# Kernel tuning notes

Measured on AMD Instinct MI355X. Metric: run time of the kernel, lower is better.

The kernel has to match this reference:

```python
import jax, jax.numpy as jnp
import numpy as np

B, S, D = 2, 2048, 2048
H, KV, HD = 16, 4, 128          # n_heads, n_kv_heads, head_dim = d_model // n_heads
R = H // KV                      # n_rep (GQA group size)
THETA = 500000.0


def _rotate_half(x):
    x1, x2 = jnp.split(x, 2, axis=-1)
    return jnp.concatenate([-x2, x1], axis=-1)


def _rope_cos_sin(position_ids):
    # inv_freq over even dims, outer with positions, duplicated (LLaMA-style)
    inv_freq = 1.0 / (THETA ** (jnp.arange(0, HD, 2, dtype=jnp.float32) / HD))
    freqs = position_ids.astype(jnp.float32)[..., None] * inv_freq  # (B, S, HD/2)
    emb = jnp.concatenate([freqs, freqs], axis=-1)                  # (B, S, HD)
    return jnp.cos(emb)[:, None], jnp.sin(emb)[:, None]             # (B, 1, S, HD)


def setup_inputs() -> dict:
    key = jax.random.key(0)
    ks = jax.random.split(key, 5)
    x = jax.random.normal(ks[0], (B, S, D), dtype=jnp.float32)
    wq = jax.random.normal(ks[1], (D, H * HD), dtype=jnp.float32) * (D ** -0.5)
    wk = jax.random.normal(ks[2], (D, KV * HD), dtype=jnp.float32) * (D ** -0.5)
    wv = jax.random.normal(ks[3], (D, KV * HD), dtype=jnp.float32) * (D ** -0.5)
    wo = jax.random.normal(ks[4], (H * HD, D), dtype=jnp.float32) * (D ** -0.5)
    causal = jnp.tril(jnp.ones((S, S), dtype=bool))
    attn_mask = jnp.where(causal, 0.0, -1e9).astype(jnp.float32)[None, None]  # (1,1,S,S)
    position_ids = jnp.tile(jnp.arange(S, dtype=jnp.int32)[None, :], (B, 1))
    return {"x": x, "wq": wq, "wk": wk, "wv": wv, "wo": wo,
            "attn_mask": attn_mask, "position_ids": position_ids}


def reference(x, wq, wk, wv, wo, attn_mask, position_ids):
    b, s, _ = x.shape
    # projections (bias-free Linear) + head split, (B, heads, S, HD)
    q = (x @ wq).reshape(b, s, H, HD).transpose(0, 2, 1, 3)
    k = (x @ wk).reshape(b, s, KV, HD).transpose(0, 2, 1, 3)
    v = (x @ wv).reshape(b, s, KV, HD).transpose(0, 2, 1, 3)
    cos, sin = _rope_cos_sin(position_ids)
    q = q * cos + _rotate_half(q) * sin
    k = k * cos + _rotate_half(k) * sin
    # GQA: group q heads (B, KV, R, S, HD); equivalent to repeat_interleave on K/V
    qg = q.reshape(b, KV, R, s, HD)
    scores = jnp.einsum('bgrsd,bgtd->bgrst', qg.astype(jnp.float32),
                        k.astype(jnp.float32)) / np.float32(np.sqrt(HD))
    scores = scores + attn_mask[:, :, None]          # (1,1,1,S,S) broadcast
    p = jax.nn.softmax(scores, axis=-1).astype(x.dtype)
    out = jnp.einsum('bgrst,bgtd->bgrsd', p, v)      # (B, KV, R, S, HD)
    out = out.reshape(b, H, s, HD).transpose(0, 2, 1, 3).reshape(b, s, H * HD)
    return out @ wo
```

## Files before the change

### kernel.cpp

```cpp
#include <hip/hip_runtime.h>
#include <hip/hip_bf16.h>
#include <math.h>

#define Bsz 2
#define Sq  2048
#define Dm  2048
#define Hn  16
#define KVn 4
#define HDn 128

typedef __attribute__((ext_vector_type(8))) short bf16x8;
typedef __attribute__((ext_vector_type(4))) float f32x4;

__device__ __forceinline__ short f2b(float f) {
    __hip_bfloat16 h = __float2bfloat16(f);
    return *reinterpret_cast<short*>(&h);
}
__device__ __forceinline__ float b2f(short s) {
    __hip_bfloat16 h = *reinterpret_cast<__hip_bfloat16*>(&s);
    return __bfloat162float(h);
}

__global__ __launch_bounds__(256) void f2b_kernel(
    const float* __restrict__ X, short* __restrict__ Y, int n4)
{
    int i = blockIdx.x * 256 + threadIdx.x;
    if (i >= n4) return;
    float4 v = ((const float4*)X)[i];
    short4 o;
    o.x = f2b(v.x); o.y = f2b(v.y); o.z = f2b(v.z); o.w = f2b(v.w);
    ((short4*)Y)[i] = o;
}

__global__ __launch_bounds__(256) void wconv_all_kernel(
    const float* __restrict__ wq, const float* __restrict__ wk,
    const float* __restrict__ wv, const float* __restrict__ wo,
    short* __restrict__ wqkvT, short* __restrict__ woT)
{
    __shared__ float t[32][33];
    const int n0 = blockIdx.x * 32;
    const int k0 = blockIdx.y * 32;
    const int tx = threadIdx.x, ty = threadIdx.y;

    const float* W; int Nsec, nloc; short* dst;
    if (n0 < 2048)      { W = wq; Nsec = 2048; nloc = n0;        dst = wqkvT + (size_t)n0 * Dm; }
    else if (n0 < 2560) { W = wk; Nsec = 512;  nloc = n0 - 2048; dst = wqkvT + (size_t)n0 * Dm; }
    else if (n0 < 3072) { W = wv; Nsec = 512;  nloc = n0 - 2560; dst = wqkvT + (size_t)n0 * Dm; }
    else                { W = wo; Nsec = 2048; nloc = n0 - 3072; dst = woT + (size_t)(n0 - 3072) * Dm; }

#pragma unroll
    for (int r = 0; r < 4; ++r) {
        const int row = ty + 8 * r;
        t[row][tx] = W[(size_t)(k0 + row) * Nsec + nloc + tx];
    }
    __syncthreads();
#pragma unroll
    for (int r = 0; r < 4; ++r) {
        const int row = ty + 8 * r;
        dst[(size_t)row * Dm + k0 + tx] = f2b(t[tx][row]);
    }
}

template <typename OT>
__global__ __launch_bounds__(256) void gemm_bt_kernel(
    const short* __restrict__ A, const short* __restrict__ Bt,
    OT* __restrict__ C, int M, int N, int K)
{
    __shared__ __align__(16) short As[128 * 64];
    __shared__ __align__(16) short Bs[128 * 64];

    const int tid  = threadIdx.x;
    const int w    = tid >> 6;
    const int lane = tid & 63;
    const int m16  = lane & 15;
    const int g4   = lane >> 4;
    const int wm   = w >> 1, wn = w & 1;

    const int row0 = blockIdx.y * 128;
    const int col0 = blockIdx.x * 128;

    const short* Ab = A  + (size_t)row0 * K;
    const short* Bb = Bt + (size_t)col0 * K;

    const int trow = tid >> 3;
    const int soct = (tid & 7) ^ (trow & 7);

    f32x4 acc[4][4];
#pragma unroll
    for (int i = 0; i < 4; ++i)
#pragma unroll
        for (int j = 0; j < 4; ++j) acc[i][j] = (f32x4){0.f, 0.f, 0.f, 0.f};

    for (int k0 = 0; k0 < K; k0 += 64) {
#pragma unroll
        for (int r = 0; r < 4; ++r) {
            const short* gp = Ab + (size_t)(r * 32 + trow) * K + k0 + soct * 8;
            short* lp = &As[(size_t)(r * 256 + w * 64) * 8];
            __builtin_amdgcn_global_load_lds(
                (const __attribute__((address_space(1))) void*)gp,
                (__attribute__((address_space(3))) void*)lp, 16, 0, 0);
        }
#pragma unroll
        for (int r = 0; r < 4; ++r) {
            const short* gp = Bb + (size_t)(r * 32 + trow) * K + k0 + soct * 8;
            short* lp = &Bs[(size_t)(r * 256 + w * 64) * 8];
            __builtin_amdgcn_global_load_lds(
                (const __attribute__((address_space(1))) void*)gp,
                (__attribute__((address_space(3))) void*)lp, 16, 0, 0);
        }
        __syncthreads();

#pragma unroll
        for (int kc = 0; kc < 2; ++kc) {
            bf16x8 a[4], b[4];
            const int swz = (kc * 4 + g4) ^ (m16 & 7);
#pragma unroll
            for (int s = 0; s < 4; ++s) {
                const int rowA = wm * 64 + s * 16 + m16;
                a[s] = *(const bf16x8*)&As[rowA * 64 + swz * 8];
                const int rowB = wn * 64 + s * 16 + m16;
                b[s] = *(const bf16x8*)&Bs[rowB * 64 + swz * 8];
            }
#pragma unroll
            for (int i = 0; i < 4; ++i)
#pragma unroll
                for (int j = 0; j < 4; ++j)
                    acc[i][j] = __builtin_amdgcn_mfma_f32_16x16x32_bf16(
                        a[i], b[j], acc[i][j], 0, 0, 0);
        }
        __syncthreads();
    }

#pragma unroll
    for (int i = 0; i < 4; ++i) {
        const int mbase = row0 + wm * 64 + i * 16 + g4 * 4;
#pragma unroll
        for (int j = 0; j < 4; ++j) {
            const int n = col0 + wn * 64 + j * 16 + m16;
#pragma unroll
            for (int r = 0; r < 4; ++r) {
                if constexpr (sizeof(OT) == 2)
                    C[(size_t)(mbase + r) * N + n] = f2b(acc[i][j][r]);
                else
                    C[(size_t)(mbase + r) * N + n] = acc[i][j][r];
            }
        }
    }
}

__global__ __launch_bounds__(256) void rope_all_kernel(
    const short* __restrict__ C3b, short* __restrict__ Qb, short* __restrict__ Kb,
    const int* __restrict__ pos_ids, float qscale, int total)
{
    int idx = blockIdx.x * blockDim.x + threadIdx.x;
    if (idx >= total) return;
    const int i = idx & 63;
    int rest = idx >> 6;
    const int s  = rest % Sq; rest /= Sq;
    const int hh = rest % 20;
    const int b  = rest / 20;

    const bool isQ = hh < 16;
    const int h      = isQ ? hh : hh - 16;
    const int colOff = isQ ? 0 : 2048;
    const int NHx    = isQ ? Hn : KVn;
    const float scale = isQ ? qscale : 1.0f;
    short* Y = isQ ? Qb : Kb;

    const int pos = pos_ids[b * Sq + s];
    const float e   = -(float)(2 * i) * (1.0f / (float)HDn);
    const float inv = powf(500000.0f, e);
    const float f   = (float)pos * inv;
    const float c   = cosf(f);
    const float sn  = sinf(f);

    const short* src = C3b + ((size_t)(b * Sq + s)) * 3072 + colOff + h * HDn;
    const float x1 = b2f(src[i]);
    const float x2 = b2f(src[i + 64]);
    const size_t dst = (((size_t)b * NHx + h) * Sq + s) * HDn;
    Y[dst + i]      = f2b((x1 * c - x2 * sn) * scale);
    Y[dst + i + 64] = f2b((x2 * c + x1 * sn) * scale);
}

__global__ __launch_bounds__(256) void vconv_kernel(
    const short* __restrict__ C3b, short* __restrict__ Vt)
{
    __shared__ short t[32][34];
    const int bk = blockIdx.z;
    const int b  = bk >> 2, kv = bk & 3;
    const int s0 = blockIdx.x * 32;
    const int d0 = blockIdx.y * 32;
    const int tx = threadIdx.x, ty = threadIdx.y;

#pragma unroll
    for (int r = 0; r < 4; ++r) {
        const int row = ty + 8 * r;
        t[row][tx] = C3b[((size_t)(b * Sq + s0 + row)) * 3072 + 2560 + kv * HDn + d0 + tx];
    }
    __syncthreads();
#pragma unroll
    for (int r = 0; r < 4; ++r) {
        const int row = ty + 8 * r;
        Vt[((size_t)bk * HDn + d0 + row) * Sq + s0 + tx] = t[tx][row];
    }
}

__global__ __launch_bounds__(256, 2) void fattn_kernel(
    const short* __restrict__ Qb, const short* __restrict__ Kb,
    const short* __restrict__ Vtb, short* __restrict__ AOb)
{
    __shared__ __align__(16) short Ks[2][64 * 128];
    __shared__ __align__(16) short Vs[2][128 * 64];

    const int tid  = threadIdx.x;
    const int w    = tid >> 6;
    const int lane = tid & 63;
    const int m16  = lane & 15;
    const int g4   = lane >> 4;

    const int i    = blockIdx.x;
    const int half = i >> 8;
    const int k4   = i & 15;
    const int qt   = half ? k4 : 15 - k4;
    const int bh   = i >> 4;
    const int h    = bh & 15;
    const int b    = bh >> 4;
    const int kv   = h >> 2;
    const int q0   = qt << 7;
    const int qA   = q0 + w * 16;
    const int qB   = q0 + 64 + w * 16;

    bf16x8 qf[2][4];
#pragma unroll
    for (int j = 0; j < 2; ++j) {
        const short* qp = Qb + (((size_t)b * Hn + h) * Sq + (j ? qB : qA) + m16) * HDn + g4 * 8;
#pragma unroll
        for (int c = 0; c < 4; ++c) qf[j][c] = *(const bf16x8*)(qp + c * 32);
    }

    const short* kbase = Kb  + ((size_t)b * KVn + kv) * Sq * HDn;
    const short* vbase = Vtb + ((size_t)b * KVn + kv) * (size_t)HDn * Sq;

    const short* gpK[4];
    const short* gpV[4];
#pragma unroll
    for (int r = 0; r < 4; ++r) {
        const int ci = r * 256 + tid;
        const int R  = ci >> 4, o = ci & 15;
        const int hf = (R >> 5) & 1, Rl = R & 31;
        const int phys = hf * 32 + ((Rl >> 2) & 3) * 8 + ((Rl >> 4) & 1) * 4 + (Rl & 3);
        gpK[r] = kbase + (size_t)phys * HDn + (o ^ (R & 7)) * 8;
        const int d = ci >> 3, ov = ci & 7;
        gpV[r] = vbase + (size_t)d * Sq + (ov ^ (d & 7)) * 8;
    }

    f32x4 Ot[2][8];
#pragma unroll
    for (int j = 0; j < 2; ++j)
#pragma unroll
        for (int t = 0; t < 8; ++t) Ot[j][t] = (f32x4){0.f, 0.f, 0.f, 0.f};
    float mcur[2] = {-1e30f, -1e30f}, lcur[2] = {0.f, 0.f};

    const int nch = qt * 2 + 2;

    auto stage = [&](int ch, int buf) {
        const size_t kt = (size_t)(ch << 6);
#pragma unroll
        for (int r = 0; r < 4; ++r) {
            const short* gp = gpK[r] + kt * HDn;
            short* lp = &Ks[buf][(size_t)(r * 256 + w * 64) * 8];
            __builtin_amdgcn_global_load_lds(
                (const __attribute__((address_space(1))) void*)gp,
                (__attribute__((address_space(3))) void*)lp, 16, 0, 0);
        }
#pragma unroll
        for (int r = 0; r < 4; ++r) {
            const short* gp = gpV[r] + kt;
            short* lp = &Vs[buf][(size_t)(r * 256 + w * 64) * 8];
            __builtin_amdgcn_global_load_lds(
                (const __attribute__((address_space(1))) void*)gp,
                (__attribute__((address_space(3))) void*)lp, 16, 0, 0);
        }
    };

    stage(0, 0);

    for (int ch = 0; ch < nch; ++ch) {
        const int cur = ch & 1;
        const int kt  = ch << 6;

        __syncthreads();
        if (ch + 1 < nch) stage(ch + 1, cur ^ 1);

        const bool last  = (ch == nch - 1);
        const bool diag0 = (ch == nch - 2);

        const short* KsC = Ks[cur];
        const short* VsC = Vs[cur];

        f32x4 sc0[4], sc1[4];
#pragma unroll
        for (int f = 0; f < 4; ++f) {
            f32x4 a0 = (f32x4){0.f, 0.f, 0.f, 0.f};
            f32x4 a1 = (f32x4){0.f, 0.f, 0.f, 0.f};
            const int krow = f * 16 + m16;
#pragma unroll
            for (int c = 0; c < 4; ++c) {
                bf16x8 kf = *(const bf16x8*)&KsC[krow * 128 + (((c * 4 + g4) ^ (m16 & 7)) * 8)];
                a0 = __builtin_amdgcn_mfma_f32_16x16x32_bf16(kf, qf[0][c], a0, 0, 0, 0);
                a1 = __builtin_amdgcn_mfma_f32_16x16x32_bf16(kf, qf[1][c], a1, 0, 0, 0);
            }
            sc0[f] = a0; sc1[f] = a1;
        }

        if (diag0) {
            const int qg = qA + m16;
#pragma unroll
            for (int f = 0; f < 4; ++f)
#pragma unroll
                for (int ii = 0; ii < 4; ++ii) {
                    const int kg = kt + (f >> 1) * 32 + g4 * 8 + (f & 1) * 4 + ii;
                    if (kg > qg) sc0[f][ii] = -1e30f;
                }
        }
        if (last) {
            const int qg = qB + m16;
#pragma unroll
            for (int f = 0; f < 4; ++f)
#pragma unroll
                for (int ii = 0; ii < 4; ++ii) {
                    const int kg = kt + (f >> 1) * 32 + g4 * 8 + (f & 1) * 4 + ii;
                    if (kg > qg) sc1[f][ii] = -1e30f;
                }
        }

        bf16x8 pf0[2], pf1[2];
        if (!last) {
            float mx = sc0[0][0];
#pragma unroll
            for (int f = 0; f < 4; ++f)
#pragma unroll
                for (int ii = 0; ii < 4; ++ii) mx = fmaxf(mx, sc0[f][ii]);
            mx = fmaxf(mx, __shfl_xor(mx, 16));
            mx = fmaxf(mx, __shfl_xor(mx, 32));
            const float nm = fmaxf(mcur[0], mx);
            const float alpha = exp2f(mcur[0] - nm);
            mcur[0] = nm;
            float ps = 0.f;
#pragma unroll
            for (int f = 0; f < 4; ++f)
#pragma unroll
                for (int ii = 0; ii < 4; ++ii) {
                    sc0[f][ii] = exp2f(sc0[f][ii] - nm);
                    ps += sc0[f][ii];
                }
            ps += __shfl_xor(ps, 16);
            ps += __shfl_xor(ps, 32);
            lcur[0] = lcur[0] * alpha + ps;
#pragma unroll
            for (int t = 0; t < 8; ++t)
#pragma unroll
                for (int ii = 0; ii < 4; ++ii) Ot[0][t][ii] *= alpha;
#pragma unroll
            for (int hf = 0; hf < 2; ++hf) {
                bf16x8 p;
#pragma unroll
                for (int j8 = 0; j8 < 8; ++j8)
                    p[j8] = f2b(j8 < 4 ? sc0[hf * 2][j8] : sc0[hf * 2 + 1][j8 - 4]);
                pf0[hf] = p;
            }
        }
        {
            float mx = sc1[0][0];
#pragma unroll
            for (int f = 0; f < 4; ++f)
#pragma unroll
                for (int ii = 0; ii < 4; ++ii) mx = fmaxf(mx, sc1[f][ii]);
            mx = fmaxf(mx, __shfl_xor(mx, 16));
            mx = fmaxf(mx, __shfl_xor(mx, 32));
            const float nm = fmaxf(mcur[1], mx);
            const float alpha = exp2f(mcur[1] - nm);
            mcur[1] = nm;
            float ps = 0.f;
#pragma unroll
            for (int f = 0; f < 4; ++f)
#pragma unroll
                for (int ii = 0; ii < 4; ++ii) {
                    sc1[f][ii] = exp2f(sc1[f][ii] - nm);
                    ps += sc1[f][ii];
                }
            ps += __shfl_xor(ps, 16);
            ps += __shfl_xor(ps, 32);
            lcur[1] = lcur[1] * alpha + ps;
#pragma unroll
            for (int t = 0; t < 8; ++t)
#pragma unroll
                for (int ii = 0; ii < 4; ++ii) Ot[1][t][ii] *= alpha;
#pragma unroll
            for (int hf = 0; hf < 2; ++hf) {
                bf16x8 p;
#pragma unroll
                for (int j8 = 0; j8 < 8; ++j8)
                    p[j8] = f2b(j8 < 4 ? sc1[hf * 2][j8] : sc1[hf * 2 + 1][j8 - 4]);
                pf1[hf] = p;
            }
        }

#pragma unroll
        for (int t = 0; t < 8; ++t) {
            const int d = t * 16 + m16;
            bf16x8 vfa = *(const bf16x8*)&VsC[d * 64 + ((g4 ^ (d & 7)) * 8)];
            bf16x8 vfb = *(const bf16x8*)&VsC[d * 64 + (((4 + g4) ^ (d & 7)) * 8)];
            if (!last) {
                Ot[0][t] = __builtin_amdgcn_mfma_f32_16x16x32_bf16(vfa, pf0[0], Ot[0][t], 0, 0, 0);
                Ot[0][t] = __builtin_amdgcn_mfma_f32_16x16x32_bf16(vfb, pf0[1], Ot[0][t], 0, 0, 0);
            }
            Ot[1][t] = __builtin_amdgcn_mfma_f32_16x16x32_bf16(vfa, pf1[0], Ot[1][t], 0, 0, 0);
            Ot[1][t] = __builtin_amdgcn_mfma_f32_16x16x32_bf16(vfb, pf1[1], Ot[1][t], 0, 0, 0);
        }
    }

#pragma unroll
    for (int j = 0; j < 2; ++j) {
        const float inv = 1.0f / lcur[j];
        short* op = AOb + ((size_t)b * Sq + (j ? qB : qA) + m16) * (Hn * HDn) + h * HDn + g4 * 4;
#pragma unroll
        for (int t = 0; t < 8; ++t) {
            short4 o;
            o.x = f2b(Ot[j][t][0] * inv);
            o.y = f2b(Ot[j][t][1] * inv);
            o.z = f2b(Ot[j][t][2] * inv);
            o.w = f2b(Ot[j][t][3] * inv);
            *(short4*)(op + t * 16) = o;
        }
    }
}

extern "C" void kernel_launch(void* const* d_in, const int* in_sizes, int n_in,
                              void* d_out, int out_size, void* d_ws, size_t ws_size,
                              hipStream_t stream)
{
    const float* x   = (const float*)d_in[0];
    const float* wq  = (const float*)d_in[1];
    const float* wk  = (const float*)d_in[2];
    const float* wv  = (const float*)d_in[3];
    const float* wo  = (const float*)d_in[4];
    const int* pos   = (const int*)d_in[6];
    float* out = (float*)d_out;

    const int M = Bsz * Sq;
    const size_t nX  = (size_t)M * Dm;

    short* xb    = (short*)d_ws;
    short* wqkvT = xb + nX;
    short* woT   = wqkvT + (size_t)3072 * Dm;
    short* C3b   = woT + (size_t)Dm * Dm;
    short* Qb    = C3b + (size_t)M * 3072;
    short* Kb    = Qb + nX;
    short* Vtb   = Kb + (size_t)Bsz * KVn * Sq * HDn;
    short* AOb   = Vtb + (size_t)Bsz * KVn * Sq * HDn;

    f2b_kernel<<<(nX / 4 + 255) / 256, 256, 0, stream>>>(x, xb, nX / 4);
    wconv_all_kernel<<<dim3(5120 / 32, Dm / 32), dim3(32, 8), 0, stream>>>(
        wq, wk, wv, wo, wqkvT, woT);

    gemm_bt_kernel<short><<<dim3(3072 / 128, M / 128), 256, 0, stream>>>(
        xb, wqkvT, C3b, M, 3072, Dm);

    {
        const float qscale = 0.08838834764831845f * 1.4426950408889634f;
        int tot = Bsz * (Hn + KVn) * Sq * 64;
        rope_all_kernel<<<(tot + 255) / 256, 256, 0, stream>>>(
            C3b, Qb, Kb, pos, qscale, tot);
    }
    vconv_kernel<<<dim3(Sq / 32, HDn / 32, Bsz * KVn), dim3(32, 8), 0, stream>>>(
        C3b, Vtb);

    fattn_kernel<<<Bsz * Hn * (Sq / 128), 256, 0, stream>>>(Qb, Kb, Vtb, AOb);

    gemm_bt_kernel<float><<<dim3(Dm / 128, M / 128), 256, 0, stream>>>(
        AOb, woT, out, M, Dm, Dm);
}
```

Measured before the change: 353.9 us.

## Share RoPE trig across heads, lazily rescale softmax, raise MFMA priority

The RoPE kernel now computes cos/sin once per (batch, position, freq) using exp2f and sincosf, then loops over all 16 Q heads and 4 K heads, which cuts transcendental work twenty-fold but launches fewer threads. The flash-attention online softmax skips the running-max update and the output rescale unless some row's max grows by more than 8 (log2 units), which saves exp and multiply work per chunk; this bounds intermediate values by 2^8 and stays exact after final normalization. s_setprio is raised around the MFMA blocks so waves issuing matrix ops get scheduling priority over softmax work in other waves.

```diff
diff --git a/kernel.cpp b/kernel.cpp
--- a/kernel.cpp
+++ b/kernel.cpp
@@ -156,30 +156,34 @@
     if (idx >= total) return;
     const int i = idx & 63;
     int rest = idx >> 6;
-    const int s  = rest % Sq; rest /= Sq;
-    const int hh = rest % 20;
-    const int b  = rest / 20;
-
-    const bool isQ = hh < 16;
-    const int h      = isQ ? hh : hh - 16;
-    const int colOff = isQ ? 0 : 2048;
-    const int NHx    = isQ ? Hn : KVn;
-    const float scale = isQ ? qscale : 1.0f;
-    short* Y = isQ ? Qb : Kb;
+    const int s = rest % Sq;
+    const int b = rest / Sq;
 
     const int pos = pos_ids[b * Sq + s];
     const float e   = -(float)(2 * i) * (1.0f / (float)HDn);
-    const float inv = powf(500000.0f, e);
+    const float inv = exp2f(e * 18.931568569324174f);
     const float f   = (float)pos * inv;
-    const float c   = cosf(f);
-    const float sn  = sinf(f);
-
-    const short* src = C3b + ((size_t)(b * Sq + s)) * 3072 + colOff + h * HDn;
-    const float x1 = b2f(src[i]);
-    const float x2 = b2f(src[i + 64]);
-    const size_t dst = (((size_t)b * NHx + h) * Sq + s) * HDn;
-    Y[dst + i]      = f2b((x1 * c - x2 * sn) * scale);
-    Y[dst + i + 64] = f2b((x2 * c + x1 * sn) * scale);
+    float sn, c;
+    sincosf(f, &sn, &c);
+
+    const short* src = C3b + ((size_t)(b * Sq + s)) * 3072;
+
+#pragma unroll
+    for (int h = 0; h < Hn; ++h) {
+        const float x1 = b2f(src[h * HDn + i]);
+        const float x2 = b2f(src[h * HDn + i + 64]);
+        const size_t dst = (((size_t)b * Hn + h) * Sq + s) * HDn;
+        Qb[dst + i]      = f2b((x1 * c - x2 * sn) * qscale);
+        Qb[dst + i + 64] = f2b((x2 * c + x1 * sn) * qscale);
+    }
+#pragma unroll
+    for (int h = 0; h < KVn; ++h) {
+        const float x1 = b2f(src[2048 + h * HDn + i]);
+        const float x2 = b2f(src[2048 + h * HDn + i + 64]);
+        const size_t dst = (((size_t)b * KVn + h) * Sq + s) * HDn;
+        Kb[dst + i]      = f2b(x1 * c - x2 * sn);
+        Kb[dst + i + 64] = f2b(x2 * c + x1 * sn);
+    }
 }
 
 __global__ __launch_bounds__(256) void vconv_kernel(
@@ -299,6 +303,7 @@
         const short* VsC = Vs[cur];
 
         f32x4 sc0[4], sc1[4];
+        __builtin_amdgcn_s_setprio(1);
 #pragma unroll
         for (int f = 0; f < 4; ++f) {
             f32x4 a0 = (f32x4){0.f, 0.f, 0.f, 0.f};
@@ -312,6 +317,7 @@
             }
             sc0[f] = a0; sc1[f] = a1;
         }
+        __builtin_amdgcn_s_setprio(0);
 
         if (diag0) {
             const int qg = qA + m16;
@@ -343,24 +349,27 @@
                 for (int ii = 0; ii < 4; ++ii) mx = fmaxf(mx, sc0[f][ii]);
             mx = fmaxf(mx, __shfl_xor(mx, 16));
             mx = fmaxf(mx, __shfl_xor(mx, 32));
-            const float nm = fmaxf(mcur[0], mx);
-            const float alpha = exp2f(mcur[0] - nm);
-            mcur[0] = nm;
+            if (!__all(mx <= mcur[0] + 8.0f)) {
+                const float nm = fmaxf(mcur[0], mx);
+                const float alpha = exp2f(mcur[0] - nm);
+                mcur[0] = nm;
+                lcur[0] *= alpha;
+#pragma unroll
+                for (int t = 0; t < 8; ++t)
+#pragma unroll
+                    for (int ii = 0; ii < 4; ++ii) Ot[0][t][ii] *= alpha;
+            }
             float ps = 0.f;
 #pragma unroll
             for (int f = 0; f < 4; ++f)
 #pragma unroll
                 for (int ii = 0; ii < 4; ++ii) {
-                    sc0[f][ii] = exp2f(sc0[f][ii] - nm);
+                    sc0[f][ii] = exp2f(sc0[f][ii] - mcur[0]);
                     ps += sc0[f][ii];
                 }
             ps += __shfl_xor(ps, 16);
             ps += __shfl_xor(ps, 32);
-            lcur[0] = lcur[0] * alpha + ps;
-#pragma unroll
-            for (int t = 0; t < 8; ++t)
-#pragma unroll
-                for (int ii = 0; ii < 4; ++ii) Ot[0][t][ii] *= alpha;
+            lcur[0] += ps;
 #pragma unroll
             for (int hf = 0; hf < 2; ++hf) {
                 bf16x8 p;
@@ -378,24 +387,27 @@
                 for (int ii = 0; ii < 4; ++ii) mx = fmaxf(mx, sc1[f][ii]);
             mx = fmaxf(mx, __shfl_xor(mx, 16));
             mx = fmaxf(mx, __shfl_xor(mx, 32));
-            const float nm = fmaxf(mcur[1], mx);
-            const float alpha = exp2f(mcur[1] - nm);
-            mcur[1] = nm;
+            if (!__all(mx <= mcur[1] + 8.0f)) {
+                const float nm = fmaxf(mcur[1], mx);
+                const float alpha = exp2f(mcur[1] - nm);
+                mcur[1] = nm;
+                lcur[1] *= alpha;
+#pragma unroll
+                for (int t = 0; t < 8; ++t)
+#pragma unroll
+                    for (int ii = 0; ii < 4; ++ii) Ot[1][t][ii] *= alpha;
+            }
             float ps = 0.f;
 #pragma unroll
             for (int f = 0; f < 4; ++f)
 #pragma unroll
                 for (int ii = 0; ii < 4; ++ii) {
-                    sc1[f][ii] = exp2f(sc1[f][ii] - nm);
+                    sc1[f][ii] = exp2f(sc1[f][ii] - mcur[1]);
                     ps += sc1[f][ii];
                 }
             ps += __shfl_xor(ps, 16);
             ps += __shfl_xor(ps, 32);
-            lcur[1] = lcur[1] * alpha + ps;
-#pragma unroll
-            for (int t = 0; t < 8; ++t)
-#pragma unroll
-                for (int ii = 0; ii < 4; ++ii) Ot[1][t][ii] *= alpha;
+            lcur[1] += ps;
 #pragma unroll
             for (int hf = 0; hf < 2; ++hf) {
                 bf16x8 p;
@@ -406,6 +418,7 @@
             }
         }
 
+        __builtin_amdgcn_s_setprio(1);
 #pragma unroll
         for (int t = 0; t < 8; ++t) {
             const int d = t * 16 + m16;
@@ -418,6 +431,7 @@
             Ot[1][t] = __builtin_amdgcn_mfma_f32_16x16x32_bf16(vfa, pf1[0], Ot[1][t], 0, 0, 0);
             Ot[1][t] = __builtin_amdgcn_mfma_f32_16x16x32_bf16(vfb, pf1[1], Ot[1][t], 0, 0, 0);
         }
+        __builtin_amdgcn_s_setprio(0);
     }
 
 #pragma unroll
@@ -469,7 +483,7 @@
 
     {
         const float qscale = 0.08838834764831845f * 1.4426950408889634f;
-        int tot = Bsz * (Hn + KVn) * Sq * 64;
+        int tot = Bsz * Sq * 64;
         rope_all_kernel<<<(tot + 255) / 256, 256, 0, stream>>>(
             C3b, Qb, Kb, pos, qscale, tot);
     }
```

Result: faster. 330.0 us (-6.8%).
